# Optimization experiments

Hardware: AMD Instinct MI355X
Metric: run time of the kernel (lower is better)

The kernel has to match this reference:

```python
import jax, jax.numpy as jnp
import numpy as np

B, S, D, H = 2, 2048, 1024, 16
DK = D // H


def setup_inputs() -> dict:
    key = jax.random.key(0)
    ks = jax.random.split(key, 12)
    scale = 1.0 / np.sqrt(D)
    inp = {
        "query": jax.random.normal(ks[0], (B, S, D), jnp.float32),
        "key": jax.random.normal(ks[1], (B, S, D), jnp.float32),
        "value": jax.random.normal(ks[2], (B, S, D), jnp.float32),
        "mask": jnp.broadcast_to(jnp.tril(jnp.ones((S, S), bool)), (B, S, S)),
        "Wq": jax.random.normal(ks[3], (D, D), jnp.float32) * scale,
        "bq": jnp.zeros((D,), jnp.float32),
        "Wk": jax.random.normal(ks[4], (D, D), jnp.float32) * scale,
        "bk": jnp.zeros((D,), jnp.float32),
        "Wv": jax.random.normal(ks[5], (D, D), jnp.float32) * scale,
        "bv": jnp.zeros((D,), jnp.float32),
        "Wo": jax.random.normal(ks[6], (D, D), jnp.float32) * scale,
        "bo": jnp.zeros((D,), jnp.float32),
    }
    return inp


def _split_heads(x):
    # [B, S, D] -> [B, H, S, DK]
    return x.reshape(B, S, H, DK).transpose(0, 2, 1, 3)


def reference(query, key, value, mask, Wq, bq, Wk, bk, Wv, bv, Wo, bo):
    q = _split_heads(query @ Wq + bq)
    k = _split_heads(key @ Wk + bk)
    v = _split_heads(value @ Wv + bv)
    # scores: [B, H, S, S]
    scores = jnp.einsum("bhqd,bhkd->bhqk", q, k) / jnp.sqrt(jnp.float32(DK))
    scores = jnp.where(mask[:, None, :, :], scores, jnp.float32(-1e9))
    p_attn = jax.nn.softmax(scores, axis=-1)
    x = jnp.einsum("bhqk,bhkd->bhqd", p_attn, v)  # [B, H, S, DK]
    x = x.transpose(0, 2, 1, 3).reshape(B, S, D)
    return x @ Wo + bo
```

## Files before the change

kernel.cpp:

```cpp
#include <hip/hip_runtime.h>


#define S_LEN 2048
#define DMODEL 1024
#define NHEAD 16
#define DKH 64
#define QSCALE 0.18033688011112042f

typedef __attribute__((ext_vector_type(8))) short short8;
typedef __attribute__((ext_vector_type(4))) float f32x4;
typedef __attribute__((ext_vector_type(4))) unsigned short ushort4v;

__device__ __forceinline__ unsigned short f2bf(float f) {
  union { float f; unsigned int u; } v; v.f = f;
  unsigned int r = v.u + 0x7fffu + ((v.u >> 16) & 1u);
  return (unsigned short)(r >> 16);
}

__device__ __forceinline__ unsigned int cvtpk_bf16(float lo, float hi) {
  unsigned int d;
  asm("v_cvt_pk_bf16_f32 %0, %1, %2" : "=v"(d) : "v"(lo), "v"(hi));
  return d;
}

__device__ __forceinline__ void gload_lds16(const void* g, void* l) {
  __builtin_amdgcn_global_load_lds(
      (const __attribute__((address_space(1))) void*)g,
      (__attribute__((address_space(3))) void*)l, 16, 0, 0);
}

__global__ __launch_bounds__(256) void transpose_cast4(
    const float* __restrict__ W0, const float* __restrict__ W1,
    const float* __restrict__ W2, const float* __restrict__ W3,
    unsigned short* __restrict__ T0, unsigned short* __restrict__ T1,
    unsigned short* __restrict__ T2, unsigned short* __restrict__ T3) {
  __shared__ float tile[32][33];
  const int z = blockIdx.z;
  const float* W = (z == 0) ? W0 : (z == 1) ? W1 : (z == 2) ? W2 : W3;
  unsigned short* Wt = (z == 0) ? T0 : (z == 1) ? T1 : (z == 2) ? T2 : T3;
  const int tx = threadIdx.x, ty = threadIdx.y;
  const int c0 = blockIdx.x * 32, r0 = blockIdx.y * 32;
#pragma unroll
  for (int i = 0; i < 32; i += 8)
    tile[ty + i][tx] = W[(r0 + ty + i) * 1024 + c0 + tx];
  __syncthreads();
#pragma unroll
  for (int i = 0; i < 32; i += 8)
    Wt[(c0 + ty + i) * 1024 + r0 + tx] = f2bf(tile[tx][ty + i]);
}

__global__ __launch_bounds__(256) void cast3(const float* __restrict__ s0,
                                             const float* __restrict__ s1,
                                             const float* __restrict__ s2,
                                             unsigned short* __restrict__ d0,
                                             unsigned short* __restrict__ d1,
                                             unsigned short* __restrict__ d2) {
  const int z = blockIdx.y;
  const float* src = (z == 0) ? s0 : (z == 1) ? s1 : s2;
  unsigned short* dst = (z == 0) ? d0 : (z == 1) ? d1 : d2;
  const int i = (blockIdx.x * 256 + threadIdx.x) * 8;
  float4 a = *(const float4*)&src[i];
  float4 b = *(const float4*)&src[i + 4];
  unsigned short u[8];
  u[0] = f2bf(a.x); u[1] = f2bf(a.y); u[2] = f2bf(a.z); u[3] = f2bf(a.w);
  u[4] = f2bf(b.x); u[5] = f2bf(b.y); u[6] = f2bf(b.z); u[7] = f2bf(b.w);
  *(short8*)&dst[i] = *(short8*)u;
}

__global__ __launch_bounds__(256) void qkv_gemm(
    const unsigned short* Qc, const unsigned short* Kc, const unsigned short* Vc,
    const unsigned short* WtQ, const unsigned short* WtK, const unsigned short* WtV,
    const float* bq, const float* bk, const float* bv,
    unsigned short* Qw, unsigned short* Kw, unsigned short* Vtw) {
  __shared__ unsigned short Alds[2][4096];
  __shared__ unsigned short Blds[2][4096];
  const int z = blockIdx.z;
  const unsigned short* A  = (z == 0) ? Qc : (z == 1) ? Kc : Vc;
  const unsigned short* Wt = (z == 0) ? WtQ : (z == 1) ? WtK : WtV;
  const float* bias        = (z == 0) ? bq : (z == 1) ? bk : bv;

  const int tid = threadIdx.x;
  const int m0 = blockIdx.x * 128, n0 = blockIdx.y * 128;
  const int wid = tid >> 6, lane = tid & 63;
  const int lg = lane >> 4, lr = lane & 15;
  const int wr = (wid >> 1) * 64, wc = (wid & 1) * 64;
  const int srow_base = wid * 32 + (lane >> 2);
  const int scol = (lane & 3) * 8;
  const int rsw = ((lr >> 1) & 3) << 3;

  f32x4 acc[4][4] = {};

#define GSTAGE(BUF, KT)                                                          \
  {                                                                              \
    _Pragma("unroll")                                                            \
    for (int i = 0; i < 2; i++) {                                                \
      const int row = srow_base + i * 16;                                        \
      const int sc = scol ^ (((row >> 1) & 3) << 3);                             \
      gload_lds16(A  + (m0 + row) * 1024 + (KT) + sc,                            \
                  (char*)&Alds[BUF][0] + wid * 2048 + i * 1024);                 \
      gload_lds16(Wt + (n0 + row) * 1024 + (KT) + sc,                            \
                  (char*)&Blds[BUF][0] + wid * 2048 + i * 1024);                 \
    }                                                                            \
  }

  GSTAGE(0, 0)
  int cur = 0;
  for (int kt = 0; kt < 1024; kt += 32) {
    __syncthreads();
    if (kt + 32 < 1024) GSTAGE(cur ^ 1, kt + 32)
    short8 af[4], bfr[4];
#pragma unroll
    for (int i = 0; i < 4; i++)
      af[i] = *(short8*)&Alds[cur][(wr + i * 16 + lr) * 32 + ((lg * 8) ^ rsw)];
#pragma unroll
    for (int i = 0; i < 4; i++)
      bfr[i] = *(short8*)&Blds[cur][(wc + i * 16 + lr) * 32 + ((lg * 8) ^ rsw)];
#pragma unroll
    for (int mi = 0; mi < 4; mi++)
#pragma unroll
      for (int ni = 0; ni < 4; ni++)
        acc[mi][ni] = __builtin_amdgcn_mfma_f32_16x16x32_bf16(af[mi], bfr[ni], acc[mi][ni], 0, 0, 0);
    cur ^= 1;
  }
#undef GSTAGE

  if (z < 2) {
    unsigned short* O = (z == 0) ? Qw : Kw;
    const float sc = (z == 0) ? QSCALE : 1.0f;
#pragma unroll
    for (int mi = 0; mi < 4; mi++)
#pragma unroll
      for (int ni = 0; ni < 4; ni++) {
        const int gn = n0 + wc + ni * 16 + lr;
        const int h = gn >> 6, dk = gn & 63;
        const float bb = bias[gn];
#pragma unroll
        for (int r = 0; r < 4; r++) {
          const int gm = m0 + wr + mi * 16 + lg * 4 + r;
          const int b = gm >> 11, s = gm & 2047;
          O[(((b * NHEAD + h) * S_LEN + s) << 6) + dk] = f2bf((acc[mi][ni][r] + bb) * sc);
        }
      }
  } else {
#pragma unroll
    for (int mi = 0; mi < 4; mi++)
#pragma unroll
      for (int ni = 0; ni < 4; ni++) {
        const int gn = n0 + wc + ni * 16 + lr;
        const int h = gn >> 6, dk = gn & 63;
        const float bb = bias[gn];
        const int gm = m0 + wr + mi * 16 + lg * 4;
        const int b = gm >> 11, s = gm & 2047;
        const int s6 = s & 63;
        const int np = (s & ~63) + ((s6 >> 5) << 5) + (((s6 >> 2) & 3) << 3) +
                       (((s6 >> 4) & 1) << 2);
        unsigned short u[4];
#pragma unroll
        for (int r = 0; r < 4; r++) u[r] = f2bf(acc[mi][ni][r] + bb);
        *(ushort4v*)&Vtw[(((b * NHEAD + h) * DKH + dk) << 11) + np] = *(ushort4v*)u;
      }
  }
}

__global__ __launch_bounds__(256) void oproj_gemm(const unsigned short* __restrict__ A,
                                                  const unsigned short* __restrict__ Wt,
                                                  const float* __restrict__ bias,
                                                  float* __restrict__ Of32) {
  __shared__ unsigned short Alds[2][2048];
  __shared__ unsigned short Blds[2][4096];
  const int tid = threadIdx.x;
  const int m0 = blockIdx.x * 64, n0 = blockIdx.y * 128;
  const int wid = tid >> 6, lane = tid & 63;
  const int lg = lane >> 4, lr = lane & 15;
  const int wc = wid * 32;
  const int arow = wid * 16 + (lane >> 2);
  const int brow_base = wid * 32 + (lane >> 2);
  const int scol = (lane & 3) * 8;
  const int rsw = ((lr >> 1) & 3) << 3;

  f32x4 acc[4][2] = {};

#define OSTAGE(BUF, KT)                                                          \
  {                                                                              \
    {                                                                            \
      const int sca = scol ^ (((arow >> 1) & 3) << 3);                           \
      gload_lds16(A + (m0 + arow) * 1024 + (KT) + sca,                           \
                  (char*)&Alds[BUF][0] + wid * 1024);                            \
    }                                                                            \
    _Pragma("unroll")                                                            \
    for (int i = 0; i < 2; i++) {                                                \
      const int row = brow_base + i * 16;                                        \
      const int scb = scol ^ (((row >> 1) & 3) << 3);                            \
      gload_lds16(Wt + (n0 + row) * 1024 + (KT) + scb,                           \
                  (char*)&Blds[BUF][0] + wid * 2048 + i * 1024);                 \
    }                                                                            \
  }

  OSTAGE(0, 0)
  int cur = 0;
  for (int kt = 0; kt < 1024; kt += 32) {
    __syncthreads();
    if (kt + 32 < 1024) OSTAGE(cur ^ 1, kt + 32)
    short8 af[4], bfr[2];
#pragma unroll
    for (int i = 0; i < 4; i++)
      af[i] = *(short8*)&Alds[cur][(i * 16 + lr) * 32 + ((lg * 8) ^ rsw)];
#pragma unroll
    for (int j = 0; j < 2; j++)
      bfr[j] = *(short8*)&Blds[cur][(wc + j * 16 + lr) * 32 + ((lg * 8) ^ rsw)];
#pragma unroll
    for (int mi = 0; mi < 4; mi++)
#pragma unroll
      for (int ni = 0; ni < 2; ni++)
        acc[mi][ni] = __builtin_amdgcn_mfma_f32_16x16x32_bf16(af[mi], bfr[ni], acc[mi][ni], 0, 0, 0);
    cur ^= 1;
  }
#undef OSTAGE

#pragma unroll
  for (int mi = 0; mi < 4; mi++)
#pragma unroll
    for (int ni = 0; ni < 2; ni++) {
      const int gn = n0 + wc + ni * 16 + lr;
      const float bb = bias[gn];
#pragma unroll
      for (int r = 0; r < 4; r++) {
        const int gm = m0 + mi * 16 + lg * 4 + r;
        Of32[gm * 1024 + gn] = acc[mi][ni][r] + bb;
      }
    }
}

__global__ __launch_bounds__(256) void attn_k(const unsigned short* __restrict__ Q,
                                              const unsigned short* __restrict__ K,
                                              const unsigned short* __restrict__ Vt,
                                              unsigned short* __restrict__ X) {
  __shared__ unsigned short Kb[2][4096];
  __shared__ unsigned short Vb[2][4096];
  const int tid = threadIdx.x;
  const int wid = tid >> 6, lane = tid & 63;
  const int lg = lane >> 4, lr = lane & 15;
  const int bh = blockIdx.y;
  const unsigned short* Qh = Q + bh * (S_LEN * DKH);
  const char* KhB = (const char*)(K + bh * (S_LEN * DKH));
  const char* VtB = (const char*)(Vt + bh * (DKH * S_LEN));
  const int b = bh >> 4, h = bh & 15;

  const int srow_lo = (lane >> 3);
  const int scolb = (lane & 7) * 16;

  short8 ones8;
#pragma unroll
  for (int i = 0; i < 8; i++) ones8[i] = (short)0x3F80;

  for (int pass = 0; pass < 2; ++pass) {
    const int qt = (pass == 0) ? (int)blockIdx.x : 31 - (int)blockIdx.x;
    const int qr = qt * 64 + wid * 16;

    short8 qf[2];
#pragma unroll
    for (int c = 0; c < 2; c++) qf[c] = *(const short8*)&Qh[(qr + lr) * 64 + c * 32 + lg * 8];

    f32x4 o[4] = {};
    f32x4 lsv = {};

    int cur = 0;
    __syncthreads();

#define STAGE(BUF, KV)                                                          \
    {                                                                           \
      _Pragma("unroll")                                                         \
      for (int i = 0; i < 2; i++) {                                             \
        const int row = wid * 16 + i * 8 + srow_lo;                             \
        const int sw = scolb ^ ((row & 7) << 4);                                \
        gload_lds16(KhB + ((KV) + row) * 128 + sw,                              \
                    (char*)&Kb[BUF][0] + wid * 2048 + i * 1024);                \
        gload_lds16(VtB + row * 4096 + (KV) * 2 + sw,                           \
                    (char*)&Vb[BUF][0] + wid * 2048 + i * 1024);                \
      }                                                                         \
    }

    STAGE(cur, 0);

    for (int t = 0; t <= qt; ++t) {
      __syncthreads();
      if (t < qt) STAGE(cur ^ 1, (t + 1) * 64);
      const bool diag = (t == qt);

      f32x4 sa[4] = {};
      __builtin_amdgcn_s_setprio(1);
#pragma unroll
      for (int jf = 0; jf < 4; jf++) {
        const int row = jf * 16 + lr;
#pragma unroll
        for (int c = 0; c < 2; c++) {
          const int cb = (c * 64 + lg * 16) ^ ((lr & 7) << 4);
          short8 kf = *(const short8*)((const char*)&Kb[cur][0] + row * 128 + cb);
          sa[jf] = __builtin_amdgcn_mfma_f32_16x16x32_bf16(kf, qf[c], sa[jf], 0, 0, 0);
        }
      }
      __builtin_amdgcn_s_setprio(0);

      float p[4][4];
      if (diag) {
        const int qloc = wid * 16 + lr;
#pragma unroll
        for (int jf = 0; jf < 4; jf++)
#pragma unroll
          for (int r = 0; r < 4; r++) {
            const float e = __builtin_amdgcn_exp2f(sa[jf][r]);
            p[jf][r] = (jf * 16 + lg * 4 + r > qloc) ? 0.f : e;
          }
      } else {
#pragma unroll
        for (int jf = 0; jf < 4; jf++)
#pragma unroll
          for (int r = 0; r < 4; r++) p[jf][r] = __builtin_amdgcn_exp2f(sa[jf][r]);
      }

      union { short8 v; unsigned int u[4]; } pk[2];
#pragma unroll
      for (int c = 0; c < 2; c++) {
        pk[c].u[0] = cvtpk_bf16(p[2 * c][0], p[2 * c][1]);
        pk[c].u[1] = cvtpk_bf16(p[2 * c][2], p[2 * c][3]);
        pk[c].u[2] = cvtpk_bf16(p[2 * c + 1][0], p[2 * c + 1][1]);
        pk[c].u[3] = cvtpk_bf16(p[2 * c + 1][2], p[2 * c + 1][3]);
      }

      __builtin_amdgcn_s_setprio(1);
#pragma unroll
      for (int f = 0; f < 4; f++) {
        const char* vrow = (const char*)&Vb[cur][0] + (f * 16 + lr) * 128;
        const int swz = (lr & 7) << 4;
#pragma unroll
        for (int c = 0; c < 2; c++) {
          short8 vf = *(const short8*)(vrow + ((c * 64 + lg * 16) ^ swz));
          o[f] = __builtin_amdgcn_mfma_f32_16x16x32_bf16(pk[c].v, vf, o[f], 0, 0, 0);
        }
      }
#pragma unroll
      for (int c = 0; c < 2; c++)
        lsv = __builtin_amdgcn_mfma_f32_16x16x32_bf16(pk[c].v, ones8, lsv, 0, 0, 0);
      __builtin_amdgcn_s_setprio(0);
      cur ^= 1;
    }

#pragma unroll
    for (int r = 0; r < 4; r++) {
      const float inv = 1.f / lsv[r];
      const int q = qr + lg * 4 + r;
#pragma unroll
      for (int f = 0; f < 4; f++)
        X[(b * S_LEN + q) * DMODEL + h * DKH + f * 16 + lr] = f2bf(o[f][r] * inv);
    }
  }
#undef STAGE
}

extern "C" void kernel_launch(void* const* d_in, const int* in_sizes, int n_in,
                              void* d_out, int out_size, void* d_ws, size_t ws_size,
                              hipStream_t stream) {
  const float* query = (const float*)d_in[0];
  const float* key   = (const float*)d_in[1];
  const float* value = (const float*)d_in[2];
  const float* Wq = (const float*)d_in[4];
  const float* bq = (const float*)d_in[5];
  const float* Wk = (const float*)d_in[6];
  const float* bk = (const float*)d_in[7];
  const float* Wv = (const float*)d_in[8];
  const float* bv = (const float*)d_in[9];
  const float* Wo = (const float*)d_in[10];
  const float* bo = (const float*)d_in[11];
  float* out = (float*)d_out;

  unsigned short* ws = (unsigned short*)d_ws;
  unsigned short* WtQ = ws;
  unsigned short* WtK = ws + 1048576;
  unsigned short* WtV = ws + 2097152;
  unsigned short* WtO = ws + 3145728;
  unsigned short* Qw  = ws + 4194304;
  unsigned short* Kw  = ws + 8388608;
  unsigned short* Vtw = ws + 12582912;
  unsigned short* Xw  = ws + 16777216;
  unsigned short* Qc  = ws + 20971520;
  unsigned short* Kc  = ws + 25165824;
  unsigned short* Vc  = ws + 29360128;
  (void)in_sizes; (void)n_in; (void)out_size; (void)ws_size;

  transpose_cast4<<<dim3(32, 32, 4), dim3(32, 8), 0, stream>>>(
      Wq, Wk, Wv, Wo, WtQ, WtK, WtV, WtO);

  cast3<<<dim3(2048, 3), 256, 0, stream>>>(query, key, value, Qc, Kc, Vc);

  qkv_gemm<<<dim3(32, 8, 3), 256, 0, stream>>>(Qc, Kc, Vc, WtQ, WtK, WtV,
                                               bq, bk, bv, Qw, Kw, Vtw);

  attn_k<<<dim3(16, 32), 256, 0, stream>>>(Qw, Kw, Vtw, Xw);

  oproj_gemm<<<dim3(64, 8), 256, 0, stream>>>(Xw, WtO, bo, out);
}
```

Baseline: 126.1 us.

## Triple-buffer LDS in QKV and output projection GEMMs with partial vmcnt waits

Switches both projection GEMMs from double to triple buffering in LDS, issuing global-to-LDS loads two K-steps ahead. A partial s_waitcnt vmcnt replaces the full __syncthreads drain, so one stage of loads can stay in flight while the current tile is computed. This hides more global memory latency but raises LDS use per block, which may lower occupancy. Correctness depends on the vmcnt counts matching the number of loads issued per stage.

```diff
diff --git a/kernel.cpp b/kernel.cpp
--- a/kernel.cpp
+++ b/kernel.cpp
@@ -72,8 +72,8 @@
     const unsigned short* WtQ, const unsigned short* WtK, const unsigned short* WtV,
     const float* bq, const float* bk, const float* bv,
     unsigned short* Qw, unsigned short* Kw, unsigned short* Vtw) {
-  __shared__ unsigned short Alds[2][4096];
-  __shared__ unsigned short Blds[2][4096];
+  __shared__ unsigned short Alds[3][4096];
+  __shared__ unsigned short Blds[3][4096];
   const int z = blockIdx.z;
   const unsigned short* A  = (z == 0) ? Qc : (z == 1) ? Kc : Vc;
   const unsigned short* Wt = (z == 0) ? WtQ : (z == 1) ? WtK : WtV;
@@ -104,23 +104,27 @@
   }
 
   GSTAGE(0, 0)
-  int cur = 0;
-  for (int kt = 0; kt < 1024; kt += 32) {
-    __syncthreads();
-    if (kt + 32 < 1024) GSTAGE(cur ^ 1, kt + 32)
+  GSTAGE(1, 32)
+  for (int t = 0; t < 32; ++t) {
+    if (t < 31) { asm volatile("s_waitcnt vmcnt(4)" ::: "memory"); }
+    else        { asm volatile("s_waitcnt vmcnt(0)" ::: "memory"); }
+    __builtin_amdgcn_s_barrier();
+    asm volatile("" ::: "memory");
+    if (t + 2 < 32) GSTAGE((t + 2) % 3, (t + 2) * 32)
+    const unsigned short* Ac = &Alds[t % 3][0];
+    const unsigned short* Bc = &Blds[t % 3][0];
     short8 af[4], bfr[4];
 #pragma unroll
     for (int i = 0; i < 4; i++)
-      af[i] = *(short8*)&Alds[cur][(wr + i * 16 + lr) * 32 + ((lg * 8) ^ rsw)];
+      af[i] = *(const short8*)&Ac[(wr + i * 16 + lr) * 32 + ((lg * 8) ^ rsw)];
 #pragma unroll
     for (int i = 0; i < 4; i++)
-      bfr[i] = *(short8*)&Blds[cur][(wc + i * 16 + lr) * 32 + ((lg * 8) ^ rsw)];
+      bfr[i] = *(const short8*)&Bc[(wc + i * 16 + lr) * 32 + ((lg * 8) ^ rsw)];
 #pragma unroll
     for (int mi = 0; mi < 4; mi++)
 #pragma unroll
       for (int ni = 0; ni < 4; ni++)
         acc[mi][ni] = __builtin_amdgcn_mfma_f32_16x16x32_bf16(af[mi], bfr[ni], acc[mi][ni], 0, 0, 0);
-    cur ^= 1;
   }
 #undef GSTAGE
 
@@ -166,8 +170,8 @@
                                                   const unsigned short* __restrict__ Wt,
                                                   const float* __restrict__ bias,
                                                   float* __restrict__ Of32) {
-  __shared__ unsigned short Alds[2][2048];
-  __shared__ unsigned short Blds[2][4096];
+  __shared__ unsigned short Alds[3][2048];
+  __shared__ unsigned short Blds[3][4096];
   const int tid = threadIdx.x;
   const int m0 = blockIdx.x * 64, n0 = blockIdx.y * 128;
   const int wid = tid >> 6, lane = tid & 63;
@@ -197,23 +201,27 @@
   }
 
   OSTAGE(0, 0)
-  int cur = 0;
-  for (int kt = 0; kt < 1024; kt += 32) {
-    __syncthreads();
-    if (kt + 32 < 1024) OSTAGE(cur ^ 1, kt + 32)
+  OSTAGE(1, 32)
+  for (int t = 0; t < 32; ++t) {
+    if (t < 31) { asm volatile("s_waitcnt vmcnt(3)" ::: "memory"); }
+    else        { asm volatile("s_waitcnt vmcnt(0)" ::: "memory"); }
+    __builtin_amdgcn_s_barrier();
+    asm volatile("" ::: "memory");
+    if (t + 2 < 32) OSTAGE((t + 2) % 3, (t + 2) * 32)
+    const unsigned short* Ac = &Alds[t % 3][0];
+    const unsigned short* Bc = &Blds[t % 3][0];
     short8 af[4], bfr[2];
 #pragma unroll
     for (int i = 0; i < 4; i++)
-      af[i] = *(short8*)&Alds[cur][(i * 16 + lr) * 32 + ((lg * 8) ^ rsw)];
+      af[i] = *(const short8*)&Ac[(i * 16 + lr) * 32 + ((lg * 8) ^ rsw)];
 #pragma unroll
     for (int j = 0; j < 2; j++)
-      bfr[j] = *(short8*)&Blds[cur][(wc + j * 16 + lr) * 32 + ((lg * 8) ^ rsw)];
+      bfr[j] = *(const short8*)&Bc[(wc + j * 16 + lr) * 32 + ((lg * 8) ^ rsw)];
 #pragma unroll
     for (int mi = 0; mi < 4; mi++)
 #pragma unroll
       for (int ni = 0; ni < 2; ni++)
         acc[mi][ni] = __builtin_amdgcn_mfma_f32_16x16x32_bf16(af[mi], bfr[ni], acc[mi][ni], 0, 0, 0);
-    cur ^= 1;
   }
 #undef OSTAGE
 
```

Measured after the change: 124.6 us. Within noise of the previous version (-1.2%).

## Fuse fp32-to-bf16 input cast into QKV GEMM A-tile loading

Applied to the files above, without the earlier changes.

Removes the separate cast3 kernel and has qkv_gemm read fp32 activations directly, converting them to bf16 in registers and writing them swizzled into LDS after the MFMA compute of each k-step. This removes one kernel launch and a full write-then-read round trip of the bf16 activation copies. In exchange the GEMM reads twice the A bytes from global memory and uses register-staged loads instead of direct global-to-LDS loads, which adds register pressure and VALU work inside the main loop.

```diff
diff --git a/kernel.cpp b/kernel.cpp
--- a/kernel.cpp
+++ b/kernel.cpp
@@ -49,33 +49,15 @@
     Wt[(c0 + ty + i) * 1024 + r0 + tx] = f2bf(tile[tx][ty + i]);
 }
 
-__global__ __launch_bounds__(256) void cast3(const float* __restrict__ s0,
-                                             const float* __restrict__ s1,
-                                             const float* __restrict__ s2,
-                                             unsigned short* __restrict__ d0,
-                                             unsigned short* __restrict__ d1,
-                                             unsigned short* __restrict__ d2) {
-  const int z = blockIdx.y;
-  const float* src = (z == 0) ? s0 : (z == 1) ? s1 : s2;
-  unsigned short* dst = (z == 0) ? d0 : (z == 1) ? d1 : d2;
-  const int i = (blockIdx.x * 256 + threadIdx.x) * 8;
-  float4 a = *(const float4*)&src[i];
-  float4 b = *(const float4*)&src[i + 4];
-  unsigned short u[8];
-  u[0] = f2bf(a.x); u[1] = f2bf(a.y); u[2] = f2bf(a.z); u[3] = f2bf(a.w);
-  u[4] = f2bf(b.x); u[5] = f2bf(b.y); u[6] = f2bf(b.z); u[7] = f2bf(b.w);
-  *(short8*)&dst[i] = *(short8*)u;
-}
-
 __global__ __launch_bounds__(256) void qkv_gemm(
-    const unsigned short* Qc, const unsigned short* Kc, const unsigned short* Vc,
+    const float* Qf, const float* Kf, const float* Vf,
     const unsigned short* WtQ, const unsigned short* WtK, const unsigned short* WtV,
     const float* bq, const float* bk, const float* bv,
     unsigned short* Qw, unsigned short* Kw, unsigned short* Vtw) {
   __shared__ unsigned short Alds[2][4096];
   __shared__ unsigned short Blds[2][4096];
   const int z = blockIdx.z;
-  const unsigned short* A  = (z == 0) ? Qc : (z == 1) ? Kc : Vc;
+  const float* A           = (z == 0) ? Qf : (z == 1) ? Kf : Vf;
   const unsigned short* Wt = (z == 0) ? WtQ : (z == 1) ? WtK : WtV;
   const float* bias        = (z == 0) ? bq : (z == 1) ? bk : bv;
 
@@ -89,25 +71,54 @@
   const int rsw = ((lr >> 1) & 3) << 3;
 
   f32x4 acc[4][4] = {};
-
-#define GSTAGE(BUF, KT)                                                          \
+  float4 a4[2][2];
+
+#define AISSUE(KT)                                                               \
+  {                                                                              \
+    _Pragma("unroll")                                                            \
+    for (int i = 0; i < 2; i++) {                                                \
+      const float* src = A + (m0 + srow_base + i * 16) * 1024 + (KT) + scol;     \
+      a4[i][0] = *(const float4*)src;                                            \
+      a4[i][1] = *(const float4*)(src + 4);                                      \
+    }                                                                            \
+  }
+
+#define AWRITE(BUF)                                                              \
+  {                                                                              \
+    _Pragma("unroll")                                                            \
+    for (int i = 0; i < 2; i++) {                                                \
+      const int row = srow_base + i * 16;                                        \
+      const int dcol = scol ^ (((row >> 1) & 3) << 3);                           \
+      union { short8 v; unsigned int u[4]; } pk;                                 \
+      pk.u[0] = cvtpk_bf16(a4[i][0].x, a4[i][0].y);                              \
+      pk.u[1] = cvtpk_bf16(a4[i][0].z, a4[i][0].w);                              \
+      pk.u[2] = cvtpk_bf16(a4[i][1].x, a4[i][1].y);                              \
+      pk.u[3] = cvtpk_bf16(a4[i][1].z, a4[i][1].w);                              \
+      *(short8*)&Alds[BUF][row * 32 + dcol] = pk.v;                              \
+    }                                                                            \
+  }
+
+#define BSTAGE(BUF, KT)                                                          \
   {                                                                              \
     _Pragma("unroll")                                                            \
     for (int i = 0; i < 2; i++) {                                                \
       const int row = srow_base + i * 16;                                        \
       const int sc = scol ^ (((row >> 1) & 3) << 3);                             \
-      gload_lds16(A  + (m0 + row) * 1024 + (KT) + sc,                            \
-                  (char*)&Alds[BUF][0] + wid * 2048 + i * 1024);                 \
       gload_lds16(Wt + (n0 + row) * 1024 + (KT) + sc,                            \
                   (char*)&Blds[BUF][0] + wid * 2048 + i * 1024);                 \
     }                                                                            \
   }
 
-  GSTAGE(0, 0)
+  AISSUE(0)
+  BSTAGE(0, 0)
+  AWRITE(0)
   int cur = 0;
   for (int kt = 0; kt < 1024; kt += 32) {
     __syncthreads();
-    if (kt + 32 < 1024) GSTAGE(cur ^ 1, kt + 32)
+    if (kt + 32 < 1024) {
+      AISSUE(kt + 32)
+      BSTAGE(cur ^ 1, kt + 32)
+    }
     short8 af[4], bfr[4];
 #pragma unroll
     for (int i = 0; i < 4; i++)
@@ -120,9 +131,12 @@
 #pragma unroll
       for (int ni = 0; ni < 4; ni++)
         acc[mi][ni] = __builtin_amdgcn_mfma_f32_16x16x32_bf16(af[mi], bfr[ni], acc[mi][ni], 0, 0, 0);
+    if (kt + 32 < 1024) AWRITE(cur ^ 1)
     cur ^= 1;
   }
-#undef GSTAGE
+#undef AISSUE
+#undef AWRITE
+#undef BSTAGE
 
   if (z < 2) {
     unsigned short* O = (z == 0) ? Qw : Kw;
@@ -382,17 +396,12 @@
   unsigned short* Kw  = ws + 8388608;
   unsigned short* Vtw = ws + 12582912;
   unsigned short* Xw  = ws + 16777216;
-  unsigned short* Qc  = ws + 20971520;
-  unsigned short* Kc  = ws + 25165824;
-  unsigned short* Vc  = ws + 29360128;
   (void)in_sizes; (void)n_in; (void)out_size; (void)ws_size;
 
   transpose_cast4<<<dim3(32, 32, 4), dim3(32, 8), 0, stream>>>(
       Wq, Wk, Wv, Wo, WtQ, WtK, WtV, WtO);
 
-  cast3<<<dim3(2048, 3), 256, 0, stream>>>(query, key, value, Qc, Kc, Vc);
-
-  qkv_gemm<<<dim3(32, 8, 3), 256, 0, stream>>>(Qc, Kc, Vc, WtQ, WtK, WtV,
+  qkv_gemm<<<dim3(32, 8, 3), 256, 0, stream>>>(query, key, value, WtQ, WtK, WtV,
                                                bq, bk, bv, Qw, Kw, Vtw);
 
   attn_k<<<dim3(16, 32), 256, 0, stream>>>(Qw, Kw, Vtw, Xw);
```

Measured after the change: 148.0 us. +17.4%, slower.

## Fuse fp32-to-bf16 input cast into QKV GEMM via fp32 LDS staging

Applied to the files above, without the earlier changes.

Removes the separate cast3 kernel and its bf16 copies of query/key/value. The QKV GEMM now stages fp32 A tiles directly into LDS with an XOR swizzle and converts them to bf16 with v_cvt_pk_bf16_f32 when loading MFMA fragments. This saves one launch and a full round trip of the activations through global memory. In exchange it doubles the A-tile LDS footprint and global load volume per GEMM block, and repeats the conversion work for every N tile.

```diff
diff --git a/kernel.cpp b/kernel.cpp
--- a/kernel.cpp
+++ b/kernel.cpp
@@ -49,33 +49,15 @@
     Wt[(c0 + ty + i) * 1024 + r0 + tx] = f2bf(tile[tx][ty + i]);
 }
 
-__global__ __launch_bounds__(256) void cast3(const float* __restrict__ s0,
-                                             const float* __restrict__ s1,
-                                             const float* __restrict__ s2,
-                                             unsigned short* __restrict__ d0,
-                                             unsigned short* __restrict__ d1,
-                                             unsigned short* __restrict__ d2) {
-  const int z = blockIdx.y;
-  const float* src = (z == 0) ? s0 : (z == 1) ? s1 : s2;
-  unsigned short* dst = (z == 0) ? d0 : (z == 1) ? d1 : d2;
-  const int i = (blockIdx.x * 256 + threadIdx.x) * 8;
-  float4 a = *(const float4*)&src[i];
-  float4 b = *(const float4*)&src[i + 4];
-  unsigned short u[8];
-  u[0] = f2bf(a.x); u[1] = f2bf(a.y); u[2] = f2bf(a.z); u[3] = f2bf(a.w);
-  u[4] = f2bf(b.x); u[5] = f2bf(b.y); u[6] = f2bf(b.z); u[7] = f2bf(b.w);
-  *(short8*)&dst[i] = *(short8*)u;
-}
-
 __global__ __launch_bounds__(256) void qkv_gemm(
-    const unsigned short* Qc, const unsigned short* Kc, const unsigned short* Vc,
+    const float* Qf, const float* Kf, const float* Vf,
     const unsigned short* WtQ, const unsigned short* WtK, const unsigned short* WtV,
     const float* bq, const float* bk, const float* bv,
     unsigned short* Qw, unsigned short* Kw, unsigned short* Vtw) {
-  __shared__ unsigned short Alds[2][4096];
+  __shared__ float Afds[2][4096];
   __shared__ unsigned short Blds[2][4096];
   const int z = blockIdx.z;
-  const unsigned short* A  = (z == 0) ? Qc : (z == 1) ? Kc : Vc;
+  const float* A           = (z == 0) ? Qf : (z == 1) ? Kf : Vf;
   const unsigned short* Wt = (z == 0) ? WtQ : (z == 1) ? WtK : WtV;
   const float* bias        = (z == 0) ? bq : (z == 1) ? bk : bv;
 
@@ -87,17 +69,24 @@
   const int srow_base = wid * 32 + (lane >> 2);
   const int scol = (lane & 3) * 8;
   const int rsw = ((lr >> 1) & 3) << 3;
+  const int arow_lo = wid * 8 + (lane >> 3);
+  const int agr = lane & 7;
 
   f32x4 acc[4][4] = {};
 
 #define GSTAGE(BUF, KT)                                                          \
   {                                                                              \
+    _Pragma("unroll")                                                            \
+    for (int i = 0; i < 4; i++) {                                                \
+      const int row = i * 32 + arow_lo;                                          \
+      const int sg = agr ^ (row & 7);                                            \
+      gload_lds16(A + (m0 + row) * 1024 + (KT) + sg * 4,                         \
+                  (char*)&Afds[BUF][0] + i * 4096 + wid * 1024);                 \
+    }                                                                            \
     _Pragma("unroll")                                                            \
     for (int i = 0; i < 2; i++) {                                                \
       const int row = srow_base + i * 16;                                        \
       const int sc = scol ^ (((row >> 1) & 3) << 3);                             \
-      gload_lds16(A  + (m0 + row) * 1024 + (KT) + sc,                            \
-                  (char*)&Alds[BUF][0] + wid * 2048 + i * 1024);                 \
       gload_lds16(Wt + (n0 + row) * 1024 + (KT) + sc,                            \
                   (char*)&Blds[BUF][0] + wid * 2048 + i * 1024);                 \
     }                                                                            \
@@ -109,9 +98,20 @@
     __syncthreads();
     if (kt + 32 < 1024) GSTAGE(cur ^ 1, kt + 32)
     short8 af[4], bfr[4];
-#pragma unroll
-    for (int i = 0; i < 4; i++)
-      af[i] = *(short8*)&Alds[cur][(wr + i * 16 + lr) * 32 + ((lg * 8) ^ rsw)];
+    const int s7 = lr & 7;
+#pragma unroll
+    for (int i = 0; i < 4; i++) {
+      const int R = wr + i * 16 + lr;
+      const char* rb = (const char*)&Afds[cur][0] + R * 128;
+      f32x4 h0 = *(const f32x4*)(rb + ((((2 * lg) ^ s7)) << 4));
+      f32x4 h1 = *(const f32x4*)(rb + ((((2 * lg + 1) ^ s7)) << 4));
+      union { short8 v; unsigned int u[4]; } pk;
+      pk.u[0] = cvtpk_bf16(h0[0], h0[1]);
+      pk.u[1] = cvtpk_bf16(h0[2], h0[3]);
+      pk.u[2] = cvtpk_bf16(h1[0], h1[1]);
+      pk.u[3] = cvtpk_bf16(h1[2], h1[3]);
+      af[i] = pk.v;
+    }
 #pragma unroll
     for (int i = 0; i < 4; i++)
       bfr[i] = *(short8*)&Blds[cur][(wc + i * 16 + lr) * 32 + ((lg * 8) ^ rsw)];
@@ -382,17 +382,12 @@
   unsigned short* Kw  = ws + 8388608;
   unsigned short* Vtw = ws + 12582912;
   unsigned short* Xw  = ws + 16777216;
-  unsigned short* Qc  = ws + 20971520;
-  unsigned short* Kc  = ws + 25165824;
-  unsigned short* Vc  = ws + 29360128;
   (void)in_sizes; (void)n_in; (void)out_size; (void)ws_size;
 
   transpose_cast4<<<dim3(32, 32, 4), dim3(32, 8), 0, stream>>>(
       Wq, Wk, Wv, Wo, WtQ, WtK, WtV, WtO);
 
-  cast3<<<dim3(2048, 3), 256, 0, stream>>>(query, key, value, Qc, Kc, Vc);
-
-  qkv_gemm<<<dim3(32, 8, 3), 256, 0, stream>>>(Qc, Kc, Vc, WtQ, WtK, WtV,
+  qkv_gemm<<<dim3(32, 8, 3), 256, 0, stream>>>(query, key, value, WtQ, WtK, WtV,
                                                bq, bk, bv, Qw, Kw, Vtw);
 
   attn_k<<<dim3(16, 32), 256, 0, stream>>>(Qw, Kw, Vtw, Xw);
```

New measurement: 136.6 us. +8.3%, slower.
